# Kernel optimization log

Measured on AMD Instinct MI355X. Metric: run time of the kernel, lower is better.

The kernel has to match this reference:

```python
import jax, jax.numpy as jnp
import numpy as np

N_NODES = 50000
N_EDGES = 300000
D_FEAT = 256
HIDDEN = 256
OUT = 40


def _sage_conv(x, src, dst, Wl, Wr, b):
    """PyG SAGEConv (mean aggr): out_i = mean_{j in N(i)} x_j @ Wl + x_i @ Wr + b."""
    n = x.shape[0]
    agg = jax.ops.segment_sum(x[src], dst, num_segments=n)              # [N, Din]
    cnt = jax.ops.segment_sum(jnp.ones((src.shape[0],), x.dtype), dst,
                              num_segments=n)                           # [N]
    mean = agg / jnp.maximum(cnt, 1.0)[:, None]
    return mean @ Wl + x @ Wr + b


def setup_inputs() -> dict:
    key = jax.random.key(0)
    ks = jax.random.split(key, 16)
    x = jax.random.normal(ks[0], (N_NODES, D_FEAT), dtype=jnp.float32)
    edge_index = jax.random.randint(ks[1], (2, N_EDGES), 0, N_NODES, dtype=jnp.int64)

    def lin(k, din, dout):
        return jax.random.normal(k, (din, dout), dtype=jnp.float32) * (1.0 / np.sqrt(din))

    dims = [(D_FEAT, HIDDEN), (D_FEAT, 64), (D_FEAT, 32), (32, OUT)]
    inp = {"x": x, "edge_index": edge_index}
    for i, (din, dout) in enumerate(dims, start=1):
        inp[f"Wl{i}"] = lin(ks[2 + 3 * (i - 1)], din, dout)
        inp[f"Wr{i}"] = lin(ks[3 + 3 * (i - 1)], din, dout)
        inp[f"b{i}"] = jnp.zeros((dout,), dtype=jnp.float32)
    return inp


def reference(x, edge_index, Wl1, Wr1, b1, Wl2, Wr2, b2, Wl3, Wr3, b3, Wl4, Wr4, b4):
    src, dst = edge_index[0], edge_index[1]
    # Faithful to source: sage1/sage2 outputs are overwritten (x re-fed to sage2/sage3).
    h = jax.nn.relu(_sage_conv(x, src, dst, Wl1, Wr1, b1))  # dead in original, kept for fidelity
    h = jax.nn.relu(_sage_conv(x, src, dst, Wl2, Wr2, b2))
    h = jax.nn.relu(_sage_conv(x, src, dst, Wl3, Wr3, b3))
    h = _sage_conv(h, src, dst, Wl4, Wr4, b4)
    return jax.nn.log_softmax(h, axis=1)
```

## Files before the change

kernel.cpp:

```cpp
#include <hip/hip_runtime.h>

#define N_NODES 50000
#define N_EDGES 300000
#define D_FEAT 256
#define NB_EDGES 1172
#define NB_PROJ 782

typedef __attribute__((ext_vector_type(8))) short bf16x8;
typedef __attribute__((ext_vector_type(4))) float f32x4;

__device__ __forceinline__ unsigned short f2bf(float f) {
    unsigned int u = __builtin_bit_cast(unsigned int, f);
    u += 0x7fffu + ((u >> 16) & 1u);
    return (unsigned short)(u >> 16);
}

__device__ __forceinline__ unsigned cvt2bf(float lo, float hi) {
    unsigned r;
    asm("v_cvt_pk_bf16_f32 %0, %1, %2" : "=v"(r) : "v"(lo), "v"(hi));
    return r;
}

__device__ __forceinline__ float4 bf4_to_f4(uint2 u) {
    float4 r;
    r.x = __builtin_bit_cast(float, u.x << 16);
    r.y = __builtin_bit_cast(float, u.x & 0xffff0000u);
    r.z = __builtin_bit_cast(float, u.y << 16);
    r.w = __builtin_bit_cast(float, u.y & 0xffff0000u);
    return r;
}

__global__ __launch_bounds__(256) void zero_wpack(const float* __restrict__ Wl,
        const float* __restrict__ Wr, unsigned short* __restrict__ bp,
        int4* __restrict__ hz) {
    int g = blockIdx.x * 256 + threadIdx.x;
    if (g < 12500) hz[g] = make_int4(0, 0, 0, 0);
    if (g < 2048) {
        int lane = g & 63;
        int ks = (g >> 6) & 7;
        int nt = g >> 9;
        int c = nt * 16 + (lane & 15);
        int kbase = ks * 32 + (lane >> 4) * 8;
        unsigned short o[8];
#pragma unroll
        for (int j = 0; j < 8; ++j) {
            int k = kbase + j;
            float v = (c < 32) ? Wl[k * 32 + c] : Wr[k * 32 + (c - 32)];
            o[j] = f2bf(v);
        }
        uint4 pk;
        pk.x = (unsigned)o[0] | ((unsigned)o[1] << 16);
        pk.y = (unsigned)o[2] | ((unsigned)o[3] << 16);
        pk.z = (unsigned)o[4] | ((unsigned)o[5] << 16);
        pk.w = (unsigned)o[6] | ((unsigned)o[7] << 16);
        ((uint4*)bp)[g] = pk;
    }
}

__global__ __launch_bounds__(256) void fillproj_kernel(const int* __restrict__ ei,
        int* __restrict__ hdeg, int* __restrict__ csr,
        const float* __restrict__ x, const unsigned short* __restrict__ bp,
        unsigned short* __restrict__ xl, unsigned short* __restrict__ xr) {
    __shared__ uint4 bs[2048];
    if (blockIdx.x < NB_EDGES) {
        int e = blockIdx.x * 256 + threadIdx.x;
        if (e < N_EDGES) {
            int s = ei[e], d = ei[N_EDGES + e];
            int pos = atomicAdd(&hdeg[d], 1);
            if (pos < 32) csr[d * 32 + pos] = s;
        }
        return;
    }
    const int tid = threadIdx.x;
#pragma unroll
    for (int i = 0; i < 8; ++i)
        bs[tid + i * 256] = ((const uint4*)bp)[tid + i * 256];
    __syncthreads();

    const int pb = blockIdx.x - NB_EDGES;
    const int lane = tid & 63;
    const int wv = tid >> 6;
    const int row0 = pb * 64 + wv * 16;
    const int arow = row0 + (lane & 15);
    const int kq = lane >> 4;
    const bool valid = arow < N_NODES;

    bf16x8 a[8];
    const float* xp = x + (size_t)arow * D_FEAT + kq * 8;
#pragma unroll
    for (int ks = 0; ks < 8; ++ks) {
        float4 p0, p1;
        if (valid) {
            p0 = *(const float4*)(xp + ks * 32);
            p1 = *(const float4*)(xp + ks * 32 + 4);
        } else {
            p0 = make_float4(0.f, 0.f, 0.f, 0.f);
            p1 = p0;
        }
        uint4 au;
        au.x = cvt2bf(p0.x, p0.y);
        au.y = cvt2bf(p0.z, p0.w);
        au.z = cvt2bf(p1.x, p1.y);
        au.w = cvt2bf(p1.z, p1.w);
        a[ks] = __builtin_bit_cast(bf16x8, au);
    }

    f32x4 acc[4];
#pragma unroll
    for (int nt = 0; nt < 4; ++nt) acc[nt] = (f32x4){0.f, 0.f, 0.f, 0.f};

#pragma unroll
    for (int nt = 0; nt < 4; ++nt) {
#pragma unroll
        for (int ks = 0; ks < 8; ++ks) {
            bf16x8 b = __builtin_bit_cast(bf16x8, bs[(nt * 8 + ks) * 64 + lane]);
            acc[nt] = __builtin_amdgcn_mfma_f32_16x16x32_bf16(a[ks], b, acc[nt], 0, 0, 0);
        }
    }

    const int orow = row0 + (lane >> 4) * 4;
    const int ocol = lane & 15;
#pragma unroll
    for (int nt = 0; nt < 4; ++nt) {
        unsigned short* dst = (nt < 2) ? xl : xr;
        const int cc = (nt & 1) * 16 + ocol;
#pragma unroll
        for (int i = 0; i < 4; ++i) {
            int r = orow + i;
            if (r < N_NODES) dst[(size_t)r * 32 + cc] = f2bf(acc[nt][i]);
        }
    }
}

__global__ __launch_bounds__(256) void h_gather8(const int* __restrict__ hdeg,
        const int* __restrict__ csr, const unsigned short* __restrict__ xl,
        const unsigned short* __restrict__ xr, const float* __restrict__ b3,
        unsigned short* __restrict__ h) {
    int gid = blockIdx.x * 256 + threadIdx.x;
    int n = gid >> 3, ql = gid & 7;
    if (n >= N_NODES) return;
    const int deg = hdeg[n];
    const int degS = min(deg, 32);
    const int gbase = (threadIdx.x & 63) & ~7;
    float4 sum = make_float4(0.f, 0.f, 0.f, 0.f);
    for (int b = 0; b < degS; b += 8) {
        int myidx = (b + ql < degS) ? csr[n * 32 + b + ql] : -1;
#pragma unroll
        for (int j = 0; j < 8; ++j) {
            int s = __shfl(myidx, gbase + j, 64);
            if (s >= 0) {
                float4 v = bf4_to_f4(*(const uint2*)(xl + (size_t)s * 32 + ql * 4));
                sum.x += v.x; sum.y += v.y; sum.z += v.z; sum.w += v.w;
            }
        }
    }
    const float inv = 1.0f / (float)max(deg, 1);
    float4 bxr = bf4_to_f4(*(const uint2*)(xr + (size_t)gid * 4));
    float4 bb = ((const float4*)b3)[ql];
    float4 r;
    r.x = fmaxf(fmaf(sum.x, inv, bxr.x + bb.x), 0.0f);
    r.y = fmaxf(fmaf(sum.y, inv, bxr.y + bb.y), 0.0f);
    r.z = fmaxf(fmaf(sum.z, inv, bxr.z + bb.z), 0.0f);
    r.w = fmaxf(fmaf(sum.w, inv, bxr.w + bb.w), 0.0f);
    uint2 o;
    o.x = cvt2bf(r.x, r.y);
    o.y = cvt2bf(r.z, r.w);
    *(uint2*)(h + (size_t)gid * 4) = o;
}

__global__ __launch_bounds__(256) void m4out_kernel(const int* __restrict__ hdeg,
        const int* __restrict__ csr, const unsigned short* __restrict__ h,
        const float* __restrict__ Wl4, const float* __restrict__ Wr4,
        const float* __restrict__ b4, float* __restrict__ out) {
    __shared__ float w[32][80];
    __shared__ float ex[32][65];
    const int tid = threadIdx.x;
    for (int i = tid; i < 32 * 80; i += 256) {
        int k = i / 80, c = i - k * 80;
        w[k][c] = (c < 40) ? Wl4[k * 40 + c] : Wr4[k * 40 + (c - 40)];
    }
    const int gid = blockIdx.x * 256 + tid;
    const int n = gid >> 3, ql = gid & 7;
    const int ng = tid >> 3;
    const bool valid = n < N_NODES;
    if (valid) {
        const int deg = hdeg[n];
        const int degS = min(deg, 32);
        const int gbase = (tid & 63) & ~7;
        float4 sum = make_float4(0.f, 0.f, 0.f, 0.f);
        for (int b = 0; b < degS; b += 8) {
            int myidx = (b + ql < degS) ? csr[n * 32 + b + ql] : -1;
#pragma unroll
            for (int j = 0; j < 8; ++j) {
                int s = __shfl(myidx, gbase + j, 64);
                if (s >= 0) {
                    float4 v = bf4_to_f4(*(const uint2*)(h + (size_t)s * 32 + ql * 4));
                    sum.x += v.x; sum.y += v.y; sum.z += v.z; sum.w += v.w;
                }
            }
        }
        const float inv = 1.0f / (float)max(deg, 1);
        float4 hv = bf4_to_f4(*(const uint2*)(h + (size_t)gid * 4));
        ex[ng][ql * 4 + 0] = sum.x * inv;
        ex[ng][ql * 4 + 1] = sum.y * inv;
        ex[ng][ql * 4 + 2] = sum.z * inv;
        ex[ng][ql * 4 + 3] = sum.w * inv;
        ex[ng][32 + ql * 4 + 0] = hv.x;
        ex[ng][32 + ql * 4 + 1] = hv.y;
        ex[ng][32 + ql * 4 + 2] = hv.z;
        ex[ng][32 + ql * 4 + 3] = hv.w;
    }
    __syncthreads();
    if (!valid) return;
    const int c0 = ql * 5;
    float acc[5];
#pragma unroll
    for (int c = 0; c < 5; ++c) acc[c] = b4[c0 + c];
#pragma unroll 8
    for (int k = 0; k < 32; ++k) {
        float mk = ex[ng][k];
        float hk = ex[ng][32 + k];
#pragma unroll
        for (int c = 0; c < 5; ++c)
            acc[c] += mk * w[k][c0 + c] + hk * w[k][40 + c0 + c];
    }
    float m = acc[0];
#pragma unroll
    for (int c = 1; c < 5; ++c) m = fmaxf(m, acc[c]);
#pragma unroll
    for (int off = 1; off < 8; off <<= 1) m = fmaxf(m, __shfl_xor(m, off, 8));
    float s = 0.0f;
#pragma unroll
    for (int c = 0; c < 5; ++c) s += expf(acc[c] - m);
#pragma unroll
    for (int off = 1; off < 8; off <<= 1) s += __shfl_xor(s, off, 8);
    const float ls = logf(s) + m;
    float* op = out + (size_t)n * 40 + c0;
#pragma unroll
    for (int c = 0; c < 5; ++c) op[c] = acc[c] - ls;
}

extern "C" void kernel_launch(void* const* d_in, const int* in_sizes, int n_in,
                              void* d_out, int out_size, void* d_ws, size_t ws_size,
                              hipStream_t stream) {
    const float* x   = (const float*)d_in[0];
    const int*   ei  = (const int*)d_in[1];
    const float* Wl3 = (const float*)d_in[8];
    const float* Wr3 = (const float*)d_in[9];
    const float* b3  = (const float*)d_in[10];
    const float* Wl4 = (const float*)d_in[11];
    const float* Wr4 = (const float*)d_in[12];
    const float* b4  = (const float*)d_in[13];
    float* outf = (float*)d_out;

    char* p = (char*)d_ws;
    int*   hdeg = (int*)p;      p += sizeof(int) * N_NODES;
    int*   csr  = (int*)p;      p += sizeof(int) * (size_t)N_NODES * 32;
    unsigned short* xl = (unsigned short*)p;  p += sizeof(short) * (size_t)N_NODES * 32;
    unsigned short* xr = (unsigned short*)p;  p += sizeof(short) * (size_t)N_NODES * 32;
    unsigned short* h  = (unsigned short*)p;  p += sizeof(short) * (size_t)N_NODES * 32;
    unsigned short* bpack = (unsigned short*)p;

    zero_wpack<<<49, 256, 0, stream>>>(Wl3, Wr3, bpack, (int4*)hdeg);
    fillproj_kernel<<<NB_EDGES + NB_PROJ, 256, 0, stream>>>(ei, hdeg, csr, x, bpack, xl, xr);
    h_gather8<<<(N_NODES * 8 + 255) / 256, 256, 0, stream>>>(hdeg, csr, xl, xr, b3, h);
    m4out_kernel<<<(N_NODES * 8 + 255) / 256, 256, 0, stream>>>(hdeg, csr, h, Wl4, Wr4, b4, outf);
}
```

Before: 71.33 us.

## Split projection K dimension across wave pairs with LDS reduction

The projection part of fillproj now has each block cover 32 rows instead of 64, with two waves per 16-row group each handling half of the 256-wide K dimension. Partial accumulators are reduced through shared memory before the store, and the block count doubles. The x loads are also issued before the __syncthreads that waits on the weight staging, so they overlap it. The aim is more memory-level parallelism and shorter per-wave latency in this bandwidth-bound projection, at the cost of staging the packed weights twice as many times, an extra barrier, and LDS reduction traffic.

```diff
diff --git a/kernel.cpp b/kernel.cpp
--- a/kernel.cpp
+++ b/kernel.cpp
@@ -4,7 +4,7 @@
 #define N_EDGES 300000
 #define D_FEAT 256
 #define NB_EDGES 1172
-#define NB_PROJ 782
+#define NB_PROJ2 1563
 
 typedef __attribute__((ext_vector_type(8))) short bf16x8;
 typedef __attribute__((ext_vector_type(4))) float f32x4;
@@ -62,6 +62,7 @@
         const float* __restrict__ x, const unsigned short* __restrict__ bp,
         unsigned short* __restrict__ xl, unsigned short* __restrict__ xr) {
     __shared__ uint4 bs[2048];
+    __shared__ float exs[2][16][64];
     if (blockIdx.x < NB_EDGES) {
         int e = blockIdx.x * 256 + threadIdx.x;
         if (e < N_EDGES) {
@@ -75,33 +76,34 @@
 #pragma unroll
     for (int i = 0; i < 8; ++i)
         bs[tid + i * 256] = ((const uint4*)bp)[tid + i * 256];
-    __syncthreads();
 
     const int pb = blockIdx.x - NB_EDGES;
     const int lane = tid & 63;
     const int wv = tid >> 6;
-    const int row0 = pb * 64 + wv * 16;
+    const int rg = wv >> 1, kh = wv & 1;
+    const int row0 = pb * 32 + rg * 16;
     const int arow = row0 + (lane & 15);
     const int kq = lane >> 4;
     const bool valid = arow < N_NODES;
 
-    bf16x8 a[8];
-    const float* xp = x + (size_t)arow * D_FEAT + kq * 8;
-#pragma unroll
-    for (int ks = 0; ks < 8; ++ks) {
-        float4 p0, p1;
-        if (valid) {
-            p0 = *(const float4*)(xp + ks * 32);
-            p1 = *(const float4*)(xp + ks * 32 + 4);
-        } else {
-            p0 = make_float4(0.f, 0.f, 0.f, 0.f);
-            p1 = p0;
-        }
+    const float* xp = x + (size_t)arow * D_FEAT + kh * 128 + kq * 8;
+    float4 p0[4], p1[4];
+    const float4 z4 = make_float4(0.f, 0.f, 0.f, 0.f);
+#pragma unroll
+    for (int ks = 0; ks < 4; ++ks) {
+        p0[ks] = valid ? *(const float4*)(xp + ks * 32) : z4;
+        p1[ks] = valid ? *(const float4*)(xp + ks * 32 + 4) : z4;
+    }
+    __syncthreads();
+
+    bf16x8 a[4];
+#pragma unroll
+    for (int ks = 0; ks < 4; ++ks) {
         uint4 au;
-        au.x = cvt2bf(p0.x, p0.y);
-        au.y = cvt2bf(p0.z, p0.w);
-        au.z = cvt2bf(p1.x, p1.y);
-        au.w = cvt2bf(p1.z, p1.w);
+        au.x = cvt2bf(p0[ks].x, p0[ks].y);
+        au.y = cvt2bf(p0[ks].z, p0[ks].w);
+        au.z = cvt2bf(p1[ks].x, p1[ks].y);
+        au.w = cvt2bf(p1[ks].z, p1[ks].w);
         a[ks] = __builtin_bit_cast(bf16x8, au);
     }
 
@@ -112,11 +114,26 @@
 #pragma unroll
     for (int nt = 0; nt < 4; ++nt) {
 #pragma unroll
-        for (int ks = 0; ks < 8; ++ks) {
-            bf16x8 b = __builtin_bit_cast(bf16x8, bs[(nt * 8 + ks) * 64 + lane]);
+        for (int ks = 0; ks < 4; ++ks) {
+            bf16x8 b = __builtin_bit_cast(bf16x8, bs[(nt * 8 + kh * 4 + ks) * 64 + lane]);
             acc[nt] = __builtin_amdgcn_mfma_f32_16x16x32_bf16(a[ks], b, acc[nt], 0, 0, 0);
         }
     }
+
+    if (kh == 1) {
+#pragma unroll
+        for (int nt = 0; nt < 4; ++nt)
+#pragma unroll
+            for (int c = 0; c < 4; ++c)
+                exs[rg][nt * 4 + c][lane] = acc[nt][c];
+    }
+    __syncthreads();
+    if (kh == 1) return;
+#pragma unroll
+    for (int nt = 0; nt < 4; ++nt)
+#pragma unroll
+        for (int c = 0; c < 4; ++c)
+            acc[nt][c] += exs[rg][nt * 4 + c][lane];
 
     const int orow = row0 + (lane >> 4) * 4;
     const int ocol = lane & 15;
@@ -262,7 +279,7 @@
     unsigned short* bpack = (unsigned short*)p;
 
     zero_wpack<<<49, 256, 0, stream>>>(Wl3, Wr3, bpack, (int4*)hdeg);
-    fillproj_kernel<<<NB_EDGES + NB_PROJ, 256, 0, stream>>>(ei, hdeg, csr, x, bpack, xl, xr);
+    fillproj_kernel<<<NB_EDGES + NB_PROJ2, 256, 0, stream>>>(ei, hdeg, csr, x, bpack, xl, xr);
     h_gather8<<<(N_NODES * 8 + 255) / 256, 256, 0, stream>>>(hdeg, csr, xl, xr, b3, h);
     m4out_kernel<<<(N_NODES * 8 + 255) / 256, 256, 0, stream>>>(hdeg, csr, h, Wl4, Wr4, b4, outf);
 }
```

New measurement: 87.39 us. 22.5% more time.
